# Kernel optimization log

Measured on AMD Instinct MI355X. Metric: run time of the kernel, lower is better.

Reference implementation:

```python
import jax, jax.numpy as jnp
import numpy as np

T, B = 256, 64
NTOKEN, NINP, NHID = 256, 64, 4096


def setup_inputs() -> dict:
    key = jax.random.key(0)
    k1, k2, k3, k4, k5, k6, k7 = jax.random.split(key, 7)
    tokens = jax.random.randint(k1, (T, B), 0, NTOKEN)            # [T, B] byte ids
    seq_len = jax.random.randint(k2, (B,), 1, T + 1)              # per-sample valid length in [1, T]
    s_in = 1.0 / np.sqrt(NINP)
    s_h = 1.0 / np.sqrt(NHID)
    emb_table = jax.random.normal(k3, (NTOKEN, NINP), jnp.float32)
    w_ih = jax.random.normal(k4, (4 * NHID, NINP), jnp.float32) * s_in
    w_hh = jax.random.normal(k5, (4 * NHID, NHID), jnp.float32) * s_h
    b_ih = jax.random.normal(k6, (4 * NHID,), jnp.float32) * s_h
    b_hh = jax.random.normal(k7, (4 * NHID,), jnp.float32) * s_h
    return {"tokens": tokens, "seq_len": seq_len, "emb_table": emb_table,
            "w_ih": w_ih, "w_hh": w_hh, "b_ih": b_ih, "b_hh": b_hh}


def reference(tokens, seq_len, emb_table, w_ih, w_hh, b_ih, b_hh):
    # Embedding lookup for all timesteps (dropout p=0.0 -> identity).
    emb = emb_table[tokens]                                   # [T, B, ninp]
    # Precompute input projections for every step (batched GEMM).
    x_proj = jnp.einsum('tbi,gi->tbg', emb, w_ih) + b_ih + b_hh  # [T, B, 4H]
    H = w_hh.shape[1]
    h0 = jnp.zeros((tokens.shape[1], H), x_proj.dtype)
    c0 = jnp.zeros_like(h0)
    feat0 = jnp.zeros_like(h0)

    def step(carry, inp):
        h, c, feat = carry
        xp, t = inp
        gates = xp + h @ w_hh.T                               # [B, 4H]
        i_g, f_g, g_g, o_g = jnp.split(gates, 4, axis=-1)     # torch gate order i,f,g,o
        c = jax.nn.sigmoid(f_g) * c + jax.nn.sigmoid(i_g) * jnp.tanh(g_g)
        h = jax.nn.sigmoid(o_g) * jnp.tanh(c)
        # get_valid_outs: at step t>0, keep previous feature once t >= seq_len.
        valid = (t < seq_len) | (t == 0)                      # [B]
        feat = jnp.where(valid[:, None], c, feat)
        return (h, c, feat), None

    (_, _, feat), _ = jax.lax.scan(step, (h0, c0, feat0),
                                   (x_proj, jnp.arange(x_proj.shape[0])))
    return feat                                               # [B, nhid]
```

## Files before the change

### kernel.cpp

```cpp
#include <hip/hip_runtime.h>
#include <hip/hip_bf16.h>

#define TSTEPS 256
#define BATCH  64
#define NINP   64
#define NHID   4096
#define NGATE  (4 * NHID)
#define KDIM   (NINP + NHID)
#define NCHUNK (KDIM / 32)
#define NGRP   (NGATE / 16)
#define NBLK   512

typedef __bf16 bf16x8 __attribute__((ext_vector_type(8)));
typedef float  f32x4  __attribute__((ext_vector_type(4)));
typedef unsigned short ushort_t;

__device__ __forceinline__ ushort_t f2b(float v) {
    __hip_bfloat16 h = __float2bfloat16(v);
    return *reinterpret_cast<ushort_t*>(&h);
}
__device__ __forceinline__ float sigf(float x) { return 1.f / (1.f + expf(-x)); }


__global__ void k_convert(const float* __restrict__ w_ih, const float* __restrict__ w_hh,
                          const float* __restrict__ b_ih, const float* __restrict__ b_hh,
                          ushort_t* __restrict__ Wp, float* __restrict__ bias) {
    const int grp  = blockIdx.x;
    const int bxo  = grp >> 1;
    const int half = grp & 1;
    for (int i = threadIdx.x; i < 16 * KDIM; i += 256) {
        int r = i / KDIM;
        int k = i - r * KDIM;
        int gt = half * 2 + (r >> 3);
        int j  = bxo * 8 + (r & 7);
        int g  = gt * NHID + j;
        float v = (k < NINP) ? w_ih[(size_t)g * NINP + k]
                             : w_hh[(size_t)g * NHID + (k - NINP)];
        int c = k >> 5, q = (k >> 3) & 3, e = k & 7;
        Wp[((size_t)grp * NCHUNK + c) * 512 + (q * 16 + r) * 8 + e] = f2b(v);
    }
    if (threadIdx.x < 16) {
        int r  = threadIdx.x;
        int gt = half * 2 + (r >> 3);
        int j  = bxo * 8 + (r & 7);
        int g  = gt * NHID + j;
        bias[g] = b_ih[g] + b_hh[g];
    }
}

__global__ void k_init(const int* __restrict__ tokens, const float* __restrict__ emb,
                       ushort_t* __restrict__ A0, float* __restrict__ cbuf) {
    int idx = blockIdx.x * 256 + threadIdx.x;
    if (idx < BATCH * KDIM) {
        int b = idx / KDIM, k = idx - b * KDIM;
        float v = (k < NINP) ? emb[tokens[b] * NINP + k] : 0.f;
        int c = k >> 5, q = (k >> 3) & 3, e = k & 7;
        A0[((size_t)(b >> 4) * NCHUNK + c) * 512 + (q * 16 + (b & 15)) * 8 + e] = f2b(v);
    }
    if (idx < BATCH * NHID) cbuf[idx] = 0.f;
}

__global__ __launch_bounds__(512, 4)
void k_step(int t, const ushort_t* __restrict__ Wp, const float* __restrict__ bias,
            const ushort_t* __restrict__ Ac, ushort_t* __restrict__ An,
            float* __restrict__ cbuf, float* __restrict__ out,
            const int* __restrict__ tokens, const int* __restrict__ seq_len,
            const float* __restrict__ emb) {
    const int tid  = threadIdx.x;
    const int wave = tid >> 6;
    const int lane = tid & 63;
    const int bx   = blockIdx.x;
    const int j0   = bx * 8;

    __shared__ float sbuf[BATCH][34];

    for (int i2 = tid; i2 < BATCH * 34; i2 += 512) (&sbuf[0][0])[i2] = 0.f;

    const int cstart = wave * 16 + (wave < 2 ? wave : 2);
    const int NC     = (wave < 2 ? 17 : 16);

    const ushort_t* pw0 = Wp + ((size_t)(bx * 2 + 0) * NCHUNK) * 512 + lane * 8;
    const ushort_t* pw1 = Wp + ((size_t)(bx * 2 + 1) * NCHUNK) * 512 + lane * 8;
    const ushort_t* pa0 = Ac + ((size_t)0 * NCHUNK) * 512 + lane * 8;
    const ushort_t* pa1 = Ac + ((size_t)1 * NCHUNK) * 512 + lane * 8;
    const ushort_t* pa2 = Ac + ((size_t)2 * NCHUNK) * 512 + lane * 8;
    const ushort_t* pa3 = Ac + ((size_t)3 * NCHUNK) * 512 + lane * 8;

    f32x4 acc[4][2];
    #pragma unroll
    for (int rt = 0; rt < 4; ++rt)
        #pragma unroll
        for (int g2 = 0; g2 < 2; ++g2)
            acc[rt][g2] = (f32x4){0.f, 0.f, 0.f, 0.f};

    #define LOADW(WD, cc) do {                                            \
        const size_t _o = (size_t)(cc) * 512;                             \
        WD[0] = *reinterpret_cast<const bf16x8*>(pw0 + _o);               \
        WD[1] = *reinterpret_cast<const bf16x8*>(pw1 + _o);               \
    } while (0)
    #define LOADA(AD, cc) do {                                            \
        const size_t _o = (size_t)(cc) * 512;                             \
        AD[0] = *reinterpret_cast<const bf16x8*>(pa0 + _o);               \
        AD[1] = *reinterpret_cast<const bf16x8*>(pa1 + _o);               \
        AD[2] = *reinterpret_cast<const bf16x8*>(pa2 + _o);               \
        AD[3] = *reinterpret_cast<const bf16x8*>(pa3 + _o);               \
    } while (0)
    #define DOMFMA(WD, AD) do {                                           \
        _Pragma("unroll")                                                 \
        for (int _rt = 0; _rt < 4; ++_rt) {                               \
            _Pragma("unroll")                                             \
            for (int _g2 = 0; _g2 < 2; ++_g2)                             \
                acc[_rt][_g2] = __builtin_amdgcn_mfma_f32_16x16x32_bf16(  \
                    AD[_rt], WD[_g2], acc[_rt][_g2], 0, 0, 0);            \
        }                                                                 \
    } while (0)

    bf16x8 wA[2], wB[2], xA[4], xB[4];
    LOADW(wA, cstart);        LOADA(xA, cstart);
    LOADW(wB, cstart + 1);    LOADA(xB, cstart + 1);
    int i = 0;
    for (; i + 2 < NC; i += 2) {
        DOMFMA(wA, xA);
        LOADW(wA, cstart + i + 2); LOADA(xA, cstart + i + 2);
        DOMFMA(wB, xB);
        if (i + 3 < NC) { LOADW(wB, cstart + i + 3); LOADA(xB, cstart + i + 3); }
    }
    DOMFMA(wA, xA);
    if ((NC & 1) == 0) DOMFMA(wB, xB);
    #undef LOADW
    #undef LOADA
    #undef DOMFMA

    __syncthreads();
    {
        const int n = lane & 15, q = lane >> 4;
        #pragma unroll
        for (int rt = 0; rt < 4; ++rt)
            #pragma unroll
            for (int g2 = 0; g2 < 2; ++g2)
                #pragma unroll
                for (int r = 0; r < 4; ++r)
                    atomicAdd(&sbuf[rt * 16 + q * 4 + r][g2 * 16 + n], acc[rt][g2][r]);
    }
    __syncthreads();

    {
        const int b  = lane;
        const int jl = wave;
        const int j  = j0 + jl;
        const int sl = seq_len[b];
        float ig = sbuf[b][ 0 + jl] + bias[           j];
        float fg = sbuf[b][ 8 + jl] + bias[    NHID + j];
        float gg = sbuf[b][16 + jl] + bias[2 * NHID + j];
        float og = sbuf[b][24 + jl] + bias[3 * NHID + j];
        int cidx = b * NHID + j;
        float cold = cbuf[cidx];
        float cn = sigf(fg) * cold + sigf(ig) * tanhf(gg);
        float hn = sigf(og) * tanhf(cn);
        cbuf[cidx] = cn;
        if (t == sl - 1) out[cidx] = cn;
        const int kk = NINP + j;
        const int c = kk >> 5, q2 = (kk >> 3) & 3, e = kk & 7;
        An[((size_t)(b >> 4) * NCHUNK + c) * 512 + (q2 * 16 + (b & 15)) * 8 + e] = f2b(hn);

        if (tid < 8 && (t + 1) < TSTEPS) {
            const int eb  = bx >> 3;
            const int k   = (bx & 7) * 8 + tid;
            const int tok = tokens[(t + 1) * BATCH + eb];
            const float v = emb[tok * NINP + k];
            const int c2 = k >> 5, q3 = (k >> 3) & 3, e2 = k & 7;
            An[((size_t)(eb >> 4) * NCHUNK + c2) * 512 + (q3 * 16 + (eb & 15)) * 8 + e2] = f2b(v);
        }
    }
}

extern "C" void kernel_launch(void* const* d_in, const int* in_sizes, int n_in,
                              void* d_out, int out_size, void* d_ws, size_t ws_size,
                              hipStream_t stream) {
    const int*   tokens  = (const int*)d_in[0];
    const int*   seq_len = (const int*)d_in[1];
    const float* emb     = (const float*)d_in[2];
    const float* w_ih    = (const float*)d_in[3];
    const float* w_hh    = (const float*)d_in[4];
    const float* b_ih    = (const float*)d_in[5];
    const float* b_hh    = (const float*)d_in[6];
    float* out = (float*)d_out;

    char* ws = (char*)d_ws;
    const size_t W_BYTES    = (size_t)NGRP * NCHUNK * 512 * 2;
    const size_t BIAS_BYTES = (size_t)NGATE * 4;
    const size_t C_BYTES    = (size_t)BATCH * NHID * 4;
    const size_t A_BYTES    = (size_t)4 * NCHUNK * 512 * 2;

    ushort_t* Wp   = (ushort_t*)ws;
    float*    bias = (float*)(ws + W_BYTES);
    float*    cbuf = (float*)(ws + W_BYTES + BIAS_BYTES);
    ushort_t* A0   = (ushort_t*)(ws + W_BYTES + BIAS_BYTES + C_BYTES);
    ushort_t* A1   = (ushort_t*)(ws + W_BYTES + BIAS_BYTES + C_BYTES + A_BYTES);

    k_convert<<<NGRP, 256, 0, stream>>>(w_ih, w_hh, b_ih, b_hh, Wp, bias);

    int init_elems = BATCH * KDIM;
    k_init<<<(init_elems + 255) / 256, 256, 0, stream>>>(tokens, emb, A0, cbuf);

    for (int t = 0; t < TSTEPS; ++t) {
        ushort_t* Acur  = (t & 1) ? A1 : A0;
        ushort_t* Anext = (t & 1) ? A0 : A1;
        k_step<<<NBLK, 512, 0, stream>>>(t, Wp, bias, Acur, Anext, cbuf, out,
                                         tokens, seq_len, emb);
    }
}
```

Baseline: 15.78 ms.

## Widen per-block gate tile to 16 hidden units and triple-buffer loads

Each block now computes 16 hidden units (64 gate rows) instead of 8, which halves the block count to 256 and doubles the number of MFMA outputs per activation-tile load. The weight prepack is reorganised so each block reads four contiguous gate-type groups. The load pipeline goes from double to triple buffering. In exchange it uses more registers (launch bounds relaxed to 2), leaves fewer blocks to fill the CUs, and the LDS reduction tile grows.

```diff
diff --git a/kernel.cpp b/kernel.cpp
--- a/kernel.cpp
+++ b/kernel.cpp
@@ -9,7 +9,7 @@
 #define KDIM   (NINP + NHID)
 #define NCHUNK (KDIM / 32)
 #define NGRP   (NGATE / 16)
-#define NBLK   512
+#define NBLK   256
 
 typedef __bf16 bf16x8 __attribute__((ext_vector_type(8)));
 typedef float  f32x4  __attribute__((ext_vector_type(4)));
@@ -25,25 +25,18 @@
 __global__ void k_convert(const float* __restrict__ w_ih, const float* __restrict__ w_hh,
                           const float* __restrict__ b_ih, const float* __restrict__ b_hh,
                           ushort_t* __restrict__ Wp, float* __restrict__ bias) {
-    const int grp  = blockIdx.x;
-    const int bxo  = grp >> 1;
-    const int half = grp & 1;
+    const int grp = blockIdx.x;
     for (int i = threadIdx.x; i < 16 * KDIM; i += 256) {
         int r = i / KDIM;
         int k = i - r * KDIM;
-        int gt = half * 2 + (r >> 3);
-        int j  = bxo * 8 + (r & 7);
-        int g  = gt * NHID + j;
+        int g = grp * 16 + r;
         float v = (k < NINP) ? w_ih[(size_t)g * NINP + k]
                              : w_hh[(size_t)g * NHID + (k - NINP)];
         int c = k >> 5, q = (k >> 3) & 3, e = k & 7;
         Wp[((size_t)grp * NCHUNK + c) * 512 + (q * 16 + r) * 8 + e] = f2b(v);
     }
     if (threadIdx.x < 16) {
-        int r  = threadIdx.x;
-        int gt = half * 2 + (r >> 3);
-        int j  = bxo * 8 + (r & 7);
-        int g  = gt * NHID + j;
+        int g = grp * 16 + threadIdx.x;
         bias[g] = b_ih[g] + b_hh[g];
     }
 }
@@ -60,7 +53,7 @@
     if (idx < BATCH * NHID) cbuf[idx] = 0.f;
 }
 
-__global__ __launch_bounds__(512, 4)
+__global__ __launch_bounds__(512, 2)
 void k_step(int t, const ushort_t* __restrict__ Wp, const float* __restrict__ bias,
             const ushort_t* __restrict__ Ac, ushort_t* __restrict__ An,
             float* __restrict__ cbuf, float* __restrict__ out,
@@ -70,65 +63,69 @@
     const int wave = tid >> 6;
     const int lane = tid & 63;
     const int bx   = blockIdx.x;
-    const int j0   = bx * 8;
-
-    __shared__ float sbuf[BATCH][34];
-
-    for (int i2 = tid; i2 < BATCH * 34; i2 += 512) (&sbuf[0][0])[i2] = 0.f;
+    const int j0   = bx * 16;
+
+    __shared__ float sbuf[BATCH][66];
+
+    for (int i2 = tid; i2 < BATCH * 66; i2 += 512) (&sbuf[0][0])[i2] = 0.f;
 
     const int cstart = wave * 16 + (wave < 2 ? wave : 2);
     const int NC     = (wave < 2 ? 17 : 16);
 
-    const ushort_t* pw0 = Wp + ((size_t)(bx * 2 + 0) * NCHUNK) * 512 + lane * 8;
-    const ushort_t* pw1 = Wp + ((size_t)(bx * 2 + 1) * NCHUNK) * 512 + lane * 8;
+    const ushort_t* pw0 = Wp + ((size_t)(0 * 256 + bx) * NCHUNK) * 512 + lane * 8;
+    const ushort_t* pw1 = Wp + ((size_t)(1 * 256 + bx) * NCHUNK) * 512 + lane * 8;
+    const ushort_t* pw2 = Wp + ((size_t)(2 * 256 + bx) * NCHUNK) * 512 + lane * 8;
+    const ushort_t* pw3 = Wp + ((size_t)(3 * 256 + bx) * NCHUNK) * 512 + lane * 8;
     const ushort_t* pa0 = Ac + ((size_t)0 * NCHUNK) * 512 + lane * 8;
     const ushort_t* pa1 = Ac + ((size_t)1 * NCHUNK) * 512 + lane * 8;
     const ushort_t* pa2 = Ac + ((size_t)2 * NCHUNK) * 512 + lane * 8;
     const ushort_t* pa3 = Ac + ((size_t)3 * NCHUNK) * 512 + lane * 8;
 
-    f32x4 acc[4][2];
+    f32x4 acc[4][4];
     #pragma unroll
     for (int rt = 0; rt < 4; ++rt)
         #pragma unroll
-        for (int g2 = 0; g2 < 2; ++g2)
-            acc[rt][g2] = (f32x4){0.f, 0.f, 0.f, 0.f};
-
-    #define LOADW(WD, cc) do {                                            \
+        for (int gt = 0; gt < 4; ++gt)
+            acc[rt][gt] = (f32x4){0.f, 0.f, 0.f, 0.f};
+
+    #define LOADF(WD, AD, cc) do {                                        \
         const size_t _o = (size_t)(cc) * 512;                             \
         WD[0] = *reinterpret_cast<const bf16x8*>(pw0 + _o);               \
         WD[1] = *reinterpret_cast<const bf16x8*>(pw1 + _o);               \
-    } while (0)
-    #define LOADA(AD, cc) do {                                            \
-        const size_t _o = (size_t)(cc) * 512;                             \
+        WD[2] = *reinterpret_cast<const bf16x8*>(pw2 + _o);               \
+        WD[3] = *reinterpret_cast<const bf16x8*>(pw3 + _o);               \
         AD[0] = *reinterpret_cast<const bf16x8*>(pa0 + _o);               \
         AD[1] = *reinterpret_cast<const bf16x8*>(pa1 + _o);               \
         AD[2] = *reinterpret_cast<const bf16x8*>(pa2 + _o);               \
         AD[3] = *reinterpret_cast<const bf16x8*>(pa3 + _o);               \
     } while (0)
+
     #define DOMFMA(WD, AD) do {                                           \
         _Pragma("unroll")                                                 \
         for (int _rt = 0; _rt < 4; ++_rt) {                               \
             _Pragma("unroll")                                             \
-            for (int _g2 = 0; _g2 < 2; ++_g2)                             \
-                acc[_rt][_g2] = __builtin_amdgcn_mfma_f32_16x16x32_bf16(  \
-                    AD[_rt], WD[_g2], acc[_rt][_g2], 0, 0, 0);            \
+            for (int _gt = 0; _gt < 4; ++_gt)                             \
+                acc[_rt][_gt] = __builtin_amdgcn_mfma_f32_16x16x32_bf16(  \
+                    AD[_rt], WD[_gt], acc[_rt][_gt], 0, 0, 0);            \
         }                                                                 \
     } while (0)
 
-    bf16x8 wA[2], wB[2], xA[4], xB[4];
-    LOADW(wA, cstart);        LOADA(xA, cstart);
-    LOADW(wB, cstart + 1);    LOADA(xB, cstart + 1);
+    bf16x8 wA[4], xA[4], wB[4], xB[4], wC[4], xC[4];
+    LOADF(wA, xA, cstart);
+    LOADF(wB, xB, cstart + 1);
+    LOADF(wC, xC, cstart + 2);
     int i = 0;
-    for (; i + 2 < NC; i += 2) {
-        DOMFMA(wA, xA);
-        LOADW(wA, cstart + i + 2); LOADA(xA, cstart + i + 2);
-        DOMFMA(wB, xB);
-        if (i + 3 < NC) { LOADW(wB, cstart + i + 3); LOADA(xB, cstart + i + 3); }
-    }
-    DOMFMA(wA, xA);
-    if ((NC & 1) == 0) DOMFMA(wB, xB);
-    #undef LOADW
-    #undef LOADA
+    for (; i + 5 < NC; i += 3) {
+        DOMFMA(wA, xA); LOADF(wA, xA, cstart + i + 3);
+        DOMFMA(wB, xB); LOADF(wB, xB, cstart + i + 4);
+        DOMFMA(wC, xC); LOADF(wC, xC, cstart + i + 5);
+    }
+    DOMFMA(wA, xA); if (i + 3 < NC) LOADF(wA, xA, cstart + i + 3);
+    DOMFMA(wB, xB); if (i + 4 < NC) LOADF(wB, xB, cstart + i + 4);
+    DOMFMA(wC, xC);
+    if (i + 3 < NC) DOMFMA(wA, xA);
+    if (i + 4 < NC) DOMFMA(wB, xB);
+    #undef LOADF
     #undef DOMFMA
 
     __syncthreads();
@@ -137,35 +134,37 @@
         #pragma unroll
         for (int rt = 0; rt < 4; ++rt)
             #pragma unroll
-            for (int g2 = 0; g2 < 2; ++g2)
+            for (int gt = 0; gt < 4; ++gt)
                 #pragma unroll
                 for (int r = 0; r < 4; ++r)
-                    atomicAdd(&sbuf[rt * 16 + q * 4 + r][g2 * 16 + n], acc[rt][g2][r]);
+                    atomicAdd(&sbuf[rt * 16 + q * 4 + r][gt * 16 + n], acc[rt][gt][r]);
     }
     __syncthreads();
 
     {
         const int b  = lane;
-        const int jl = wave;
-        const int j  = j0 + jl;
         const int sl = seq_len[b];
-        float ig = sbuf[b][ 0 + jl] + bias[           j];
-        float fg = sbuf[b][ 8 + jl] + bias[    NHID + j];
-        float gg = sbuf[b][16 + jl] + bias[2 * NHID + j];
-        float og = sbuf[b][24 + jl] + bias[3 * NHID + j];
-        int cidx = b * NHID + j;
-        float cold = cbuf[cidx];
-        float cn = sigf(fg) * cold + sigf(ig) * tanhf(gg);
-        float hn = sigf(og) * tanhf(cn);
-        cbuf[cidx] = cn;
-        if (t == sl - 1) out[cidx] = cn;
-        const int kk = NINP + j;
-        const int c = kk >> 5, q2 = (kk >> 3) & 3, e = kk & 7;
-        An[((size_t)(b >> 4) * NCHUNK + c) * 512 + (q2 * 16 + (b & 15)) * 8 + e] = f2b(hn);
-
-        if (tid < 8 && (t + 1) < TSTEPS) {
-            const int eb  = bx >> 3;
-            const int k   = (bx & 7) * 8 + tid;
+        #pragma unroll
+        for (int jj = 0; jj < 2; ++jj) {
+            const int jl = wave + jj * 8;
+            const int j  = j0 + jl;
+            float ig = sbuf[b][ 0 + jl] + bias[           j];
+            float fg = sbuf[b][16 + jl] + bias[    NHID + j];
+            float gg = sbuf[b][32 + jl] + bias[2 * NHID + j];
+            float og = sbuf[b][48 + jl] + bias[3 * NHID + j];
+            int cidx = b * NHID + j;
+            float cold = cbuf[cidx];
+            float cn = sigf(fg) * cold + sigf(ig) * tanhf(gg);
+            float hn = sigf(og) * tanhf(cn);
+            cbuf[cidx] = cn;
+            if (t == sl - 1) out[cidx] = cn;
+            const int kk = NINP + j;
+            const int c = kk >> 5, q2 = (kk >> 3) & 3, e = kk & 7;
+            An[((size_t)(b >> 4) * NCHUNK + c) * 512 + (q2 * 16 + (b & 15)) * 8 + e] = f2b(hn);
+        }
+        if (tid < 16 && (t + 1) < TSTEPS) {
+            const int eb  = bx >> 2;
+            const int k   = (bx & 3) * 16 + tid;
             const int tok = tokens[(t + 1) * BATCH + eb];
             const float v = emb[tok * NINP + k];
             const int c2 = k >> 5, q3 = (k >> 3) & 3, e2 = k & 7;
```

Result: slower. 16.94 ms (+7.4%).
